# Optimization experiments

Hardware: AMD Instinct MI355X
Metric: run time of the kernel (lower is better)

Reference implementation:

```python
import jax, jax.numpy as jnp
import numpy as np

B, S, HID = 4, 2048, 1024
H, DH = 16, 64  # HID = H * DH
ADP, NTASKS = 64, 10
GATE_S = 100.0  # s (soft gate temperature), != smax=400 so no hard threshold


def setup_inputs() -> dict:
    key = jax.random.key(0)
    ks = jax.random.split(key, 13)
    sc = 0.02
    return {
        "hidden_states": jax.random.normal(ks[0], (B, S, HID), jnp.float32),
        "Wq": jax.random.normal(ks[1], (HID, HID), jnp.float32) * sc,
        "bq": jax.random.normal(ks[2], (HID,), jnp.float32) * sc,
        "Wk": jax.random.normal(ks[3], (HID, HID), jnp.float32) * sc,
        "bk": jax.random.normal(ks[4], (HID,), jnp.float32) * sc,
        "Wv": jax.random.normal(ks[5], (HID, HID), jnp.float32) * sc,
        "bv": jax.random.normal(ks[6], (HID,), jnp.float32) * sc,
        "fc1_w": jax.random.normal(ks[7], (HID, ADP), jnp.float32) * sc,
        "fc1_b": jax.random.normal(ks[8], (ADP,), jnp.float32) * sc,
        "fc2_w": jax.random.normal(ks[9], (ADP, HID), jnp.float32) * sc,
        "fc2_b": jax.random.normal(ks[10], (HID,), jnp.float32) * sc,
        "efc1": jax.random.normal(ks[11], (NTASKS, ADP), jnp.float32),
        "efc2": jax.random.normal(ks[12], (NTASKS, HID), jnp.float32),
        "t": 3,
    }


def reference(hidden_states, Wq, bq, Wk, bk, Wv, bv,
              fc1_w, fc1_b, fc2_w, fc2_b, efc1, efc2, t):
    x = hidden_states
    # --- parallel adapter with task gates (add_residual=False) ---
    gfc1 = jax.nn.sigmoid(GATE_S * efc1[t])  # [ADP]
    gfc2 = jax.nn.sigmoid(GATE_S * efc2[t])  # [HID]
    h = jax.nn.relu(x @ fc1_w + fc1_b) * gfc1          # [B,S,ADP]
    adapter_out = jax.nn.relu(h @ fc2_w + fc2_b) * gfc2  # [B,S,HID]
    # --- multi-head self-attention (absolute positions, no mask, eval dropout) ---
    def split_heads(y):  # [B,S,HID] -> [B,H,S,DH]
        return y.reshape(B, S, H, DH).transpose(0, 2, 1, 3)
    q = split_heads(x @ Wq + bq)
    k = split_heads(x @ Wk + bk)
    v = split_heads(x @ Wv + bv)
    scores = jnp.einsum("bhqd,bhkd->bhqk", q, k) / np.sqrt(DH).astype(jnp.float32)
    probs = jax.nn.softmax(scores, axis=-1)
    ctx = jnp.einsum("bhqk,bhkd->bhqd", probs, v)
    ctx = ctx.transpose(0, 2, 1, 3).reshape(B, S, HID)
    return ctx + adapter_out
```

## Files before the change

### kernel.cpp

```cpp
#include <hip/hip_runtime.h>
#include <stdint.h>
#include <stddef.h>

typedef unsigned short u16;
typedef unsigned int u32;
typedef __bf16 bf16x8 __attribute__((ext_vector_type(8)));
typedef short s16x4 __attribute__((ext_vector_type(4)));
typedef float f32x4 __attribute__((ext_vector_type(4)));

#define BB  4
#define SS  2048
#define HIDD 1024
#define NH  16
#define DHD 64

#define GLD16(gaddr, laddr) \
  __builtin_amdgcn_global_load_lds( \
      (const __attribute__((address_space(1))) u32*)(gaddr), \
      (__attribute__((address_space(3))) u32*)(laddr), 16, 0, 0)

#define LDS_BARRIER() asm volatile("s_waitcnt lgkmcnt(0)\n\ts_barrier" ::: "memory")

#if __has_builtin(__builtin_amdgcn_exp2f)
  #define EXP2(x) __builtin_amdgcn_exp2f(x)
#else
  #define EXP2(x) __expf((x) * 0.6931471805599453f)
#endif

__device__ __forceinline__ u16 f2b(float f){
  union { float f; unsigned u; } c; c.f = f;
  unsigned r = c.u + 0x7fffu + ((c.u >> 16) & 1u);
  return (u16)(r >> 16);
}
__device__ __forceinline__ u16 f2b_fast(float f){
  union { float f; unsigned u; } c; c.f = f;
  return (u16)((c.u + 0x8000u) >> 16);
}
__device__ __forceinline__ f32x4 mfma32(bf16x8 a, bf16x8 b, f32x4 c){
  return __builtin_amdgcn_mfma_f32_16x16x32_bf16(a, b, c, 0, 0, 0);
}
__device__ __forceinline__ f32x4 mfma16(s16x4 a, s16x4 b, f32x4 c){
  return __builtin_amdgcn_mfma_f32_16x16x16bf16_1k(a, b, c, 0, 0, 0);
}

__global__ __launch_bounds__(256)
void prep(const float* __restrict__ x, u16* __restrict__ xb,
          const float* __restrict__ Wq, const float* __restrict__ Wk,
          const float* __restrict__ Wv, const float* __restrict__ f1w,
          const float* __restrict__ f2w,
          u16* __restrict__ wqkv, u16* __restrict__ wtf1, u16* __restrict__ wtf2)
{
  __shared__ float tile[32][33];
  int blk = blockIdx.x;
  const int tid = threadIdx.x;
  if (blk < 8192) {
    int i = blk * 1024 + tid * 4;
    float4 v = *reinterpret_cast<const float4*>(&x[i]);
    ushort4 o;
    o.x = f2b(v.x); o.y = f2b(v.y); o.z = f2b(v.z); o.w = f2b(v.w);
    *reinterpret_cast<ushort4*>(&xb[i]) = o;
    return;
  }
  blk -= 8192;
  const float* in; u16* out; int R, C, c0, r0;
  if (blk < 3072) {
    int m = blk >> 10, t = blk & 1023;
    in = (m == 0) ? Wq : (m == 1) ? Wk : Wv;
    out = wqkv + (size_t)m * 1024 * 1024;
    R = 1024; C = 1024; c0 = (t & 31) * 32; r0 = (t >> 5) * 32;
  } else if (blk < 3136) {
    int t = blk - 3072;
    in = f1w; out = wtf1; R = 1024; C = 64;
    c0 = (t & 1) * 32; r0 = (t >> 1) * 32;
  } else {
    int t = blk - 3136;
    in = f2w; out = wtf2; R = 64; C = 1024;
    c0 = (t & 31) * 32; r0 = (t >> 5) * 32;
  }
  int tx = tid & 31, ty = tid >> 5;
  #pragma unroll
  for (int j = 0; j < 32; j += 8)
    tile[ty + j][tx] = in[(size_t)(r0 + ty + j) * C + c0 + tx];
  __syncthreads();
  #pragma unroll
  for (int j = 0; j < 32; j += 8)
    out[(size_t)(c0 + ty + j) * R + r0 + tx] = f2b(tile[tx][ty + j]);
}

__global__ __launch_bounds__(256)
void gemm_qkv(const u16* __restrict__ X, const u16* __restrict__ Wt,
              const float* __restrict__ bq, const float* __restrict__ bk,
              const float* __restrict__ bv,
              u16* __restrict__ qb, u16* __restrict__ kb, u16* __restrict__ vt)
{
  constexpr int K = 1024;
  __shared__ __align__(16) u16 ldsX[128 * 32];
  __shared__ __align__(16) u16 ldsW[128 * 32];
  const int tid = threadIdx.x;
  const int w = tid >> 6, lane = tid & 63, quad = lane >> 4, ln = lane & 15;
  const int m0 = blockIdx.y * 128, n0 = blockIdx.x * 128;
  const int wrow = (w >> 1) * 64;
  const int wcol = (w & 1) * 64;
  const int srow = tid >> 2;
  const int scol = (tid & 3) * 8;

  f32x4 acc[4][4] = {};

  for (int k0 = 0; k0 < K; k0 += 32) {
    #pragma unroll
    for (int c = 0; c < 2; ++c)
      GLD16(&X[(size_t)(m0 + c * 64 + srow) * K + k0 + scol], &ldsX[c * 2048 + w * 512]);
    #pragma unroll
    for (int c = 0; c < 2; ++c)
      GLD16(&Wt[(size_t)(n0 + c * 64 + srow) * K + k0 + scol], &ldsW[c * 2048 + w * 512]);
    __syncthreads();

    bf16x8 a[4], bfr[4];
    #pragma unroll
    for (int mt = 0; mt < 4; ++mt)
      a[mt] = *reinterpret_cast<const bf16x8*>(&ldsX[(wrow + mt * 16 + ln) * 32 + quad * 8]);
    #pragma unroll
    for (int nt = 0; nt < 4; ++nt)
      bfr[nt] = *reinterpret_cast<const bf16x8*>(&ldsW[(wcol + nt * 16 + ln) * 32 + quad * 8]);
    #pragma unroll
    for (int mt = 0; mt < 4; ++mt)
      #pragma unroll
      for (int nt = 0; nt < 4; ++nt)
        acc[mt][nt] = mfma32(a[mt], bfr[nt], acc[mt][nt]);
    __syncthreads();
  }

  if (n0 < 2048) {
    const float scale = (n0 < 1024) ? 0.18033688f : 1.f;
    const float* bias = (n0 < 1024) ? bq : bk;
    u16* dst = (n0 < 1024) ? qb : kb;
    const int nb = n0 & 1023;
    #pragma unroll
    for (int nt = 0; nt < 4; ++nt) {
      const int col = nb + wcol + nt * 16 + ln;
      const float bvv = bias[col];
      #pragma unroll
      for (int mt = 0; mt < 4; ++mt)
        #pragma unroll
        for (int r = 0; r < 4; ++r) {
          int row = m0 + wrow + mt * 16 + quad * 4 + r;
          dst[(size_t)row * 1024 + col] = f2b((acc[mt][nt][r] + bvv) * scale);
        }
    }
  } else {
    #pragma unroll
    for (int nt = 0; nt < 4; ++nt) {
      const int colv = (n0 - 2048) + wcol + nt * 16 + ln;
      const float bvv = bv[colv];
      const int h = colv >> 6, d = colv & 63;
      #pragma unroll
      for (int mt = 0; mt < 4; ++mt) {
        int row = m0 + wrow + mt * 16 + quad * 4;
        int bb = row >> 11, s = row & 2047;
        ushort4 o;
        o.x = f2b(acc[mt][nt][0] + bvv);
        o.y = f2b(acc[mt][nt][1] + bvv);
        o.z = f2b(acc[mt][nt][2] + bvv);
        o.w = f2b(acc[mt][nt][3] + bvv);
        *reinterpret_cast<ushort4*>(
            &vt[((((size_t)bb * NH + h) * DHD + d) << 11) + s]) = o;
      }
    }
  }
}

template<int BM, int BN, int WR, int WC>
__global__ __launch_bounds__(256)
void gemm_bt(const u16* __restrict__ X, const u16* __restrict__ Wt,
             const float* __restrict__ bias, u16* __restrict__ outp,
             int M, int N, int K,
             const float* __restrict__ gate, const int* __restrict__ tptr)
{
  constexpr int MT = BM / (WR * 16);
  constexpr int NT = BN / (WC * 16);
  __shared__ __align__(16) u16 ldsX[BM * 32];
  __shared__ __align__(16) u16 ldsW[BN * 32];
  const int tid = threadIdx.x;
  const int w = tid >> 6, lane = tid & 63, quad = lane >> 4, ln = lane & 15;
  const int m0 = blockIdx.y * BM, n0 = blockIdx.x * BN;
  const int wrow = (w / WC) * (MT * 16);
  const int wcol = (w % WC) * (NT * 16);
  const int srow = tid >> 2;
  const int scol = (tid & 3) * 8;

  f32x4 acc[MT][NT] = {};

  for (int k0 = 0; k0 < K; k0 += 32) {
    #pragma unroll
    for (int c = 0; c < BM / 64; ++c)
      GLD16(&X[(size_t)(m0 + c * 64 + srow) * K + k0 + scol], &ldsX[c * 2048 + w * 512]);
    #pragma unroll
    for (int c = 0; c < BN / 64; ++c)
      GLD16(&Wt[(size_t)(n0 + c * 64 + srow) * K + k0 + scol], &ldsW[c * 2048 + w * 512]);
    __syncthreads();

    bf16x8 a[MT], bfr[NT];
    #pragma unroll
    for (int mt = 0; mt < MT; ++mt)
      a[mt] = *reinterpret_cast<const bf16x8*>(&ldsX[(wrow + mt * 16 + ln) * 32 + quad * 8]);
    #pragma unroll
    for (int nt = 0; nt < NT; ++nt)
      bfr[nt] = *reinterpret_cast<const bf16x8*>(&ldsW[(wcol + nt * 16 + ln) * 32 + quad * 8]);
    #pragma unroll
    for (int mt = 0; mt < MT; ++mt)
      #pragma unroll
      for (int nt = 0; nt < NT; ++nt)
        acc[mt][nt] = mfma32(a[mt], bfr[nt], acc[mt][nt]);
    __syncthreads();
  }

  int t = tptr[0];
  if ((unsigned)t > 9u) t = 0;
  #pragma unroll
  for (int nt = 0; nt < NT; ++nt) {
    const int col = n0 + wcol + nt * 16 + ln;
    const float bvv = bias[col];
    const float g = 1.f / (1.f + __expf(-100.f * gate[t * N + col]));
    #pragma unroll
    for (int mt = 0; mt < MT; ++mt) {
      #pragma unroll
      for (int r = 0; r < 4; ++r) {
        int row = m0 + wrow + mt * 16 + quad * 4 + r;
        outp[(size_t)row * N + col] = f2b(fmaxf(acc[mt][nt][r] + bvv, 0.f) * g);
      }
    }
  }
}

__global__ __launch_bounds__(256, 4)
void attn(const u16* __restrict__ Q, const u16* __restrict__ Kb,
          const u16* __restrict__ Vt, const u16* __restrict__ hb,
          const u16* __restrict__ w2, const float* __restrict__ b2,
          const float* __restrict__ gate2, const int* __restrict__ tptr,
          float* __restrict__ out)
{
  __shared__ __align__(16) u16 ldsK[64 * 72];
  __shared__ __align__(16) u16 ldsV[64 * 76];

  const int tid = threadIdx.x;
  const int w = tid >> 6, lane = tid & 63, quad = lane >> 4, ln = lane & 15;
  const int h = blockIdx.x, b = blockIdx.y, qt = blockIdx.z;
  const int bh = b * NH + h;
  const int qbase = qt * 128 + w * 32;
  const int skey = tid >> 3;
  const int sd   = (tid & 7) * 8;

  bf16x8 qf[2][2];
  #pragma unroll
  for (int q2 = 0; q2 < 2; ++q2)
    #pragma unroll
    for (int kk = 0; kk < 2; ++kk)
      qf[q2][kk] = *reinterpret_cast<const bf16x8*>(
          &Q[(size_t)(b * SS + qbase + q2 * 16 + ln) * HIDD + h * DHD + kk * 32 + quad * 8]);

  f32x4 o[4][2] = {};
  float lsum[2] = {0.f, 0.f};

  const u16* Kp = &Kb[(size_t)(b * SS + skey) * HIDD + h * DHD + sd];
  const u16* Vp = &Vt[((size_t)bh * DHD + skey) * SS + sd];

  uint4 rK0 = *reinterpret_cast<const uint4*>(Kp);
  uint4 rK1 = *reinterpret_cast<const uint4*>(Kp + (size_t)32 * HIDD);
  uint4 rV0 = *reinterpret_cast<const uint4*>(Vp);
  uint4 rV1 = *reinterpret_cast<const uint4*>(Vp + (size_t)32 * SS);

  for (int kt = 0; kt < SS; kt += 64) {
    LDS_BARRIER();
    *reinterpret_cast<uint4*>(&ldsK[skey * 72 + sd])        = rK0;
    *reinterpret_cast<uint4*>(&ldsK[(32 + skey) * 72 + sd]) = rK1;
    *reinterpret_cast<uint4*>(&ldsV[skey * 76 + sd])        = rV0;
    *reinterpret_cast<uint4*>(&ldsV[(32 + skey) * 76 + sd]) = rV1;
    if (kt + 64 < SS) {
      const u16* Kn = Kp + (size_t)(kt + 64) * HIDD;
      const u16* Vn = Vp + (kt + 64);
      rK0 = *reinterpret_cast<const uint4*>(Kn);
      rK1 = *reinterpret_cast<const uint4*>(Kn + (size_t)32 * HIDD);
      rV0 = *reinterpret_cast<const uint4*>(Vn);
      rV1 = *reinterpret_cast<const uint4*>(Vn + (size_t)32 * SS);
    }
    LDS_BARRIER();

    f32x4 s[4][2];
    #pragma unroll
    for (int k4 = 0; k4 < 4; ++k4) {
      bf16x8 kf0 = *reinterpret_cast<const bf16x8*>(&ldsK[(k4 * 16 + ln) * 72 + quad * 8]);
      bf16x8 kf1 = *reinterpret_cast<const bf16x8*>(&ldsK[(k4 * 16 + ln) * 72 + 32 + quad * 8]);
      #pragma unroll
      for (int q2 = 0; q2 < 2; ++q2) {
        f32x4 z = {0.f, 0.f, 0.f, 0.f};
        z = mfma32(kf0, qf[q2][0], z);
        z = mfma32(kf1, qf[q2][1], z);
        s[k4][q2] = z;
      }
    }

    s16x4 p[4][2];
    #pragma unroll
    for (int k4 = 0; k4 < 4; ++k4)
      #pragma unroll
      for (int q2 = 0; q2 < 2; ++q2)
        #pragma unroll
        for (int r = 0; r < 4; ++r) {
          float pv = EXP2(s[k4][q2][r]);
          lsum[q2] += pv;
          p[k4][q2][r] = (short)f2b_fast(pv);
        }

    #pragma unroll
    for (int dt = 0; dt < 4; ++dt) {
      #pragma unroll
      for (int ks = 0; ks < 4; ++ks) {
        s16x4 vf = *reinterpret_cast<const s16x4*>(
            &ldsV[(dt * 16 + ln) * 76 + ks * 16 + quad * 4]);
        #pragma unroll
        for (int q2 = 0; q2 < 2; ++q2)
          o[dt][q2] = mfma16(vf, p[ks][q2], o[dt][q2]);
      }
    }
  }

  float rl[2];
  #pragma unroll
  for (int q2 = 0; q2 < 2; ++q2) {
    float v = lsum[q2];
    v += __shfl_xor(v, 16);
    v += __shfl_xor(v, 32);
    rl[q2] = 1.f / v;
  }

  f32x4 acc2[4][2] = {};
  #pragma unroll
  for (int kk = 0; kk < 2; ++kk) {
    bf16x8 hf[2];
    #pragma unroll
    for (int q2 = 0; q2 < 2; ++q2) {
      int q = qbase + q2 * 16 + ln;
      hf[q2] = *reinterpret_cast<const bf16x8*>(
          &hb[(size_t)(b * SS + q) * 64 + kk * 32 + quad * 8]);
    }
    #pragma unroll
    for (int dt = 0; dt < 4; ++dt) {
      bf16x8 wf = *reinterpret_cast<const bf16x8*>(
          &w2[(size_t)(h * DHD + dt * 16 + ln) * 64 + kk * 32 + quad * 8]);
      #pragma unroll
      for (int q2 = 0; q2 < 2; ++q2)
        acc2[dt][q2] = mfma32(wf, hf[q2], acc2[dt][q2]);
    }
  }

  int t = tptr[0];
  if ((unsigned)t > 9u) t = 0;
  float bv2[4][4], gv2[4][4];
  #pragma unroll
  for (int dt = 0; dt < 4; ++dt)
    #pragma unroll
    for (int r = 0; r < 4; ++r) {
      int col = h * DHD + dt * 16 + quad * 4 + r;
      bv2[dt][r] = b2[col];
      gv2[dt][r] = 1.f / (1.f + __expf(-100.f * gate2[t * HIDD + col]));
    }

  #pragma unroll
  for (int q2 = 0; q2 < 2; ++q2) {
    const int q = qbase + q2 * 16 + ln;
    float* orow = &out[(size_t)(b * SS + q) * HIDD + h * DHD];
    #pragma unroll
    for (int dt = 0; dt < 4; ++dt)
      #pragma unroll
      for (int r = 0; r < 4; ++r) {
        int d = dt * 16 + quad * 4 + r;
        float ad = fmaxf(acc2[dt][q2][r] + bv2[dt][r], 0.f) * gv2[dt][r];
        orow[d] = o[dt][q2][r] * rl[q2] + ad;
      }
  }
}

extern "C" void kernel_launch(void* const* d_in, const int* in_sizes, int n_in,
                              void* d_out, int out_size, void* d_ws, size_t ws_size,
                              hipStream_t stream) {
  const float* x    = (const float*)d_in[0];
  const float* Wq   = (const float*)d_in[1];
  const float* bq   = (const float*)d_in[2];
  const float* Wk   = (const float*)d_in[3];
  const float* bk   = (const float*)d_in[4];
  const float* Wv   = (const float*)d_in[5];
  const float* bv   = (const float*)d_in[6];
  const float* f1w  = (const float*)d_in[7];
  const float* f1b  = (const float*)d_in[8];
  const float* f2w  = (const float*)d_in[9];
  const float* f2b_ = (const float*)d_in[10];
  const float* efc1 = (const float*)d_in[11];
  const float* efc2 = (const float*)d_in[12];
  const int*   tptr = (const int*)d_in[13];
  float* out = (float*)d_out;

  unsigned char* ws = (unsigned char*)d_ws;
  u16* xb   = (u16*)(ws + 0);
  u16* wqkv = (u16*)(ws + (16u << 20));
  u16* wtf1 = (u16*)(ws + (22u << 20));
  u16* wtf2 = (u16*)(ws + (22u << 20) + (128u << 10));
  u16* hb   = (u16*)(ws + (23u << 20));
  u16* qb   = (u16*)(ws + (24u << 20));
  u16* kb   = (u16*)(ws + (40u << 20));
  u16* vt   = (u16*)(ws + (56u << 20));

  prep<<<dim3(11392), 256, 0, stream>>>(x, xb, Wq, Wk, Wv, f1w, f2w,
                                        wqkv, wtf1, wtf2);

  gemm_qkv<<<dim3(24, 64), 256, 0, stream>>>(xb, wqkv, bq, bk, bv, qb, kb, vt);

  gemm_bt<64,64,2,2><<<dim3(1, 128), 256, 0, stream>>>(
      xb, wtf1, f1b, hb, 8192, 64, 1024, efc1, tptr);

  attn<<<dim3(NH, BB, SS / 128), 256, 0, stream>>>(
      qb, kb, vt, hb, wtf2, f2b_, efc2, tptr, out);
}
```

Measured before the change: 289.9 us.

## Fuse adapter fc1 into QKV GEMM and halve attention query tile per block

```diff
diff --git a/kernel.cpp b/kernel.cpp
--- a/kernel.cpp
+++ b/kernel.cpp
@@ -5,6 +5,7 @@
 typedef unsigned short u16;
 typedef unsigned int u32;
 typedef __bf16 bf16x8 __attribute__((ext_vector_type(8)));
+typedef __bf16 bf16x4 __attribute__((ext_vector_type(4)));
 typedef short s16x4 __attribute__((ext_vector_type(4)));
 typedef float f32x4 __attribute__((ext_vector_type(4)));
 
@@ -31,10 +32,6 @@
   union { float f; unsigned u; } c; c.f = f;
   unsigned r = c.u + 0x7fffu + ((c.u >> 16) & 1u);
   return (u16)(r >> 16);
-}
-__device__ __forceinline__ u16 f2b_fast(float f){
-  union { float f; unsigned u; } c; c.f = f;
-  return (u16)((c.u + 0x8000u) >> 16);
 }
 __device__ __forceinline__ f32x4 mfma32(bf16x8 a, bf16x8 b, f32x4 c){
   return __builtin_amdgcn_mfma_f32_16x16x32_bf16(a, b, c, 0, 0, 0);
@@ -62,6 +59,12 @@
     return;
   }
   blk -= 8192;
+  if (blk >= 3200) {
+    u16* pad = wqkv + (size_t)3136 * 1024;
+    uint4 z = make_uint4(0u, 0u, 0u, 0u);
+    *reinterpret_cast<uint4*>(&pad[(size_t)(blk - 3200) * 2048 + tid * 8]) = z;
+    return;
+  }
   const float* in; u16* out; int R, C, c0, r0;
   if (blk < 3072) {
     int m = blk >> 10, t = blk & 1023;
@@ -91,7 +94,10 @@
 void gemm_qkv(const u16* __restrict__ X, const u16* __restrict__ Wt,
               const float* __restrict__ bq, const float* __restrict__ bk,
               const float* __restrict__ bv,
-              u16* __restrict__ qb, u16* __restrict__ kb, u16* __restrict__ vt)
+              const float* __restrict__ f1b, const float* __restrict__ efc1,
+              const int* __restrict__ tptr,
+              u16* __restrict__ qb, u16* __restrict__ kb, u16* __restrict__ vt,
+              u16* __restrict__ hb)
 {
   constexpr int K = 1024;
   __shared__ __align__(16) u16 ldsX[128 * 32];
@@ -147,7 +153,7 @@
           dst[(size_t)row * 1024 + col] = f2b((acc[mt][nt][r] + bvv) * scale);
         }
     }
-  } else {
+  } else if (n0 < 3072) {
     #pragma unroll
     for (int nt = 0; nt < 4; ++nt) {
       const int colv = (n0 - 2048) + wcol + nt * 16 + ln;
@@ -166,73 +172,26 @@
             &vt[((((size_t)bb * NH + h) * DHD + d) << 11) + s]) = o;
       }
     }
-  }
-}
-
-template<int BM, int BN, int WR, int WC>
-__global__ __launch_bounds__(256)
-void gemm_bt(const u16* __restrict__ X, const u16* __restrict__ Wt,
-             const float* __restrict__ bias, u16* __restrict__ outp,
-             int M, int N, int K,
-             const float* __restrict__ gate, const int* __restrict__ tptr)
-{
-  constexpr int MT = BM / (WR * 16);
-  constexpr int NT = BN / (WC * 16);
-  __shared__ __align__(16) u16 ldsX[BM * 32];
-  __shared__ __align__(16) u16 ldsW[BN * 32];
-  const int tid = threadIdx.x;
-  const int w = tid >> 6, lane = tid & 63, quad = lane >> 4, ln = lane & 15;
-  const int m0 = blockIdx.y * BM, n0 = blockIdx.x * BN;
-  const int wrow = (w / WC) * (MT * 16);
-  const int wcol = (w % WC) * (NT * 16);
-  const int srow = tid >> 2;
-  const int scol = (tid & 3) * 8;
-
-  f32x4 acc[MT][NT] = {};
-
-  for (int k0 = 0; k0 < K; k0 += 32) {
-    #pragma unroll
-    for (int c = 0; c < BM / 64; ++c)
-      GLD16(&X[(size_t)(m0 + c * 64 + srow) * K + k0 + scol], &ldsX[c * 2048 + w * 512]);
-    #pragma unroll
-    for (int c = 0; c < BN / 64; ++c)
-      GLD16(&Wt[(size_t)(n0 + c * 64 + srow) * K + k0 + scol], &ldsW[c * 2048 + w * 512]);
-    __syncthreads();
-
-    bf16x8 a[MT], bfr[NT];
-    #pragma unroll
-    for (int mt = 0; mt < MT; ++mt)
-      a[mt] = *reinterpret_cast<const bf16x8*>(&ldsX[(wrow + mt * 16 + ln) * 32 + quad * 8]);
-    #pragma unroll
-    for (int nt = 0; nt < NT; ++nt)
-      bfr[nt] = *reinterpret_cast<const bf16x8*>(&ldsW[(wcol + nt * 16 + ln) * 32 + quad * 8]);
-    #pragma unroll
-    for (int mt = 0; mt < MT; ++mt)
-      #pragma unroll
-      for (int nt = 0; nt < NT; ++nt)
-        acc[mt][nt] = mfma32(a[mt], bfr[nt], acc[mt][nt]);
-    __syncthreads();
-  }
-
-  int t = tptr[0];
-  if ((unsigned)t > 9u) t = 0;
-  #pragma unroll
-  for (int nt = 0; nt < NT; ++nt) {
-    const int col = n0 + wcol + nt * 16 + ln;
-    const float bvv = bias[col];
-    const float g = 1.f / (1.f + __expf(-100.f * gate[t * N + col]));
-    #pragma unroll
-    for (int mt = 0; mt < MT; ++mt) {
-      #pragma unroll
-      for (int r = 0; r < 4; ++r) {
-        int row = m0 + wrow + mt * 16 + quad * 4 + r;
-        outp[(size_t)row * N + col] = f2b(fmaxf(acc[mt][nt][r] + bvv, 0.f) * g);
-      }
-    }
-  }
-}
-
-__global__ __launch_bounds__(256, 4)
+  } else if (wcol == 0) {
+    int t = tptr[0];
+    if ((unsigned)t > 9u) t = 0;
+    #pragma unroll
+    for (int nt = 0; nt < 4; ++nt) {
+      const int col = nt * 16 + ln;
+      const float bvv = f1b[col];
+      const float g = 1.f / (1.f + __expf(-100.f * efc1[t * 64 + col]));
+      #pragma unroll
+      for (int mt = 0; mt < 4; ++mt)
+        #pragma unroll
+        for (int r = 0; r < 4; ++r) {
+          int row = m0 + wrow + mt * 16 + quad * 4 + r;
+          hb[(size_t)row * 64 + col] = f2b(fmaxf(acc[mt][nt][r] + bvv, 0.f) * g);
+        }
+    }
+  }
+}
+
+__global__ __launch_bounds__(256, 8)
 void attn(const u16* __restrict__ Q, const u16* __restrict__ Kb,
           const u16* __restrict__ Vt, const u16* __restrict__ hb,
           const u16* __restrict__ w2, const float* __restrict__ b2,
@@ -246,20 +205,18 @@
   const int w = tid >> 6, lane = tid & 63, quad = lane >> 4, ln = lane & 15;
   const int h = blockIdx.x, b = blockIdx.y, qt = blockIdx.z;
   const int bh = b * NH + h;
-  const int qbase = qt * 128 + w * 32;
+  const int qbase = qt * 64 + w * 16;
   const int skey = tid >> 3;
   const int sd   = (tid & 7) * 8;
 
-  bf16x8 qf[2][2];
-  #pragma unroll
-  for (int q2 = 0; q2 < 2; ++q2)
-    #pragma unroll
-    for (int kk = 0; kk < 2; ++kk)
-      qf[q2][kk] = *reinterpret_cast<const bf16x8*>(
-          &Q[(size_t)(b * SS + qbase + q2 * 16 + ln) * HIDD + h * DHD + kk * 32 + quad * 8]);
-
-  f32x4 o[4][2] = {};
-  float lsum[2] = {0.f, 0.f};
+  bf16x8 qf[2];
+  #pragma unroll
+  for (int kk = 0; kk < 2; ++kk)
+    qf[kk] = *reinterpret_cast<const bf16x8*>(
+        &Q[(size_t)(b * SS + qbase + ln) * HIDD + h * DHD + kk * 32 + quad * 8]);
+
+  f32x4 o[4] = {};
+  float lsum = 0.f;
 
   const u16* Kp = &Kb[(size_t)(b * SS + skey) * HIDD + h * DHD + sd];
   const u16* Vp = &Vt[((size_t)bh * DHD + skey) * SS + sd];
@@ -285,99 +242,77 @@
     }
     LDS_BARRIER();
 
-    f32x4 s[4][2];
+    f32x4 s[4];
+    __builtin_amdgcn_s_setprio(1);
     #pragma unroll
     for (int k4 = 0; k4 < 4; ++k4) {
       bf16x8 kf0 = *reinterpret_cast<const bf16x8*>(&ldsK[(k4 * 16 + ln) * 72 + quad * 8]);
       bf16x8 kf1 = *reinterpret_cast<const bf16x8*>(&ldsK[(k4 * 16 + ln) * 72 + 32 + quad * 8]);
-      #pragma unroll
-      for (int q2 = 0; q2 < 2; ++q2) {
-        f32x4 z = {0.f, 0.f, 0.f, 0.f};
-        z = mfma32(kf0, qf[q2][0], z);
-        z = mfma32(kf1, qf[q2][1], z);
-        s[k4][q2] = z;
+      f32x4 z = {0.f, 0.f, 0.f, 0.f};
+      z = mfma32(kf0, qf[0], z);
+      z = mfma32(kf1, qf[1], z);
+      s[k4] = z;
+    }
+    __builtin_amdgcn_s_setprio(0);
+
+    s16x4 p[4];
+    #pragma unroll
+    for (int k4 = 0; k4 < 4; ++k4) {
+      union { bf16x4 b; s16x4 s; } cv;
+      #pragma unroll
+      for (int r = 0; r < 4; ++r) {
+        float pv = EXP2(s[k4][r]);
+        lsum += pv;
+        cv.b[r] = (__bf16)pv;
       }
-    }
-
-    s16x4 p[4][2];
-    #pragma unroll
-    for (int k4 = 0; k4 < 4; ++k4)
-      #pragma unroll
-      for (int q2 = 0; q2 < 2; ++q2)
-        #pragma unroll
-        for (int r = 0; r < 4; ++r) {
-          float pv = EXP2(s[k4][q2][r]);
-          lsum[q2] += pv;
-          p[k4][q2][r] = (short)f2b_fast(pv);
-        }
-
+      p[k4] = cv.s;
+    }
+
+    __builtin_amdgcn_s_setprio(1);
     #pragma unroll
     for (int dt = 0; dt < 4; ++dt) {
       #pragma unroll
       for (int ks = 0; ks < 4; ++ks) {
         s16x4 vf = *reinterpret_cast<const s16x4*>(
             &ldsV[(dt * 16 + ln) * 76 + ks * 16 + quad * 4]);
-        #pragma unroll
-        for (int q2 = 0; q2 < 2; ++q2)
-          o[dt][q2] = mfma16(vf, p[ks][q2], o[dt][q2]);
+        o[dt] = mfma16(vf, p[ks], o[dt]);
       }
     }
-  }
-
-  float rl[2];
-  #pragma unroll
-  for (int q2 = 0; q2 < 2; ++q2) {
-    float v = lsum[q2];
-    v += __shfl_xor(v, 16);
-    v += __shfl_xor(v, 32);
-    rl[q2] = 1.f / v;
-  }
-
-  f32x4 acc2[4][2] = {};
+    __builtin_amdgcn_s_setprio(0);
+  }
+
+  float v = lsum;
+  v += __shfl_xor(v, 16);
+  v += __shfl_xor(v, 32);
+  const float rl = 1.f / v;
+
+  f32x4 acc2[4] = {};
   #pragma unroll
   for (int kk = 0; kk < 2; ++kk) {
-    bf16x8 hf[2];
-    #pragma unroll
-    for (int q2 = 0; q2 < 2; ++q2) {
-      int q = qbase + q2 * 16 + ln;
-      hf[q2] = *reinterpret_cast<const bf16x8*>(
-          &hb[(size_t)(b * SS + q) * 64 + kk * 32 + quad * 8]);
-    }
+    bf16x8 hf = *reinterpret_cast<const bf16x8*>(
+        &hb[(size_t)(b * SS + qbase + ln) * 64 + kk * 32 + quad * 8]);
     #pragma unroll
     for (int dt = 0; dt < 4; ++dt) {
       bf16x8 wf = *reinterpret_cast<const bf16x8*>(
           &w2[(size_t)(h * DHD + dt * 16 + ln) * 64 + kk * 32 + quad * 8]);
-      #pragma unroll
-      for (int q2 = 0; q2 < 2; ++q2)
-        acc2[dt][q2] = mfma32(wf, hf[q2], acc2[dt][q2]);
+      acc2[dt] = mfma32(wf, hf, acc2[dt]);
     }
   }
 
   int t = tptr[0];
   if ((unsigned)t > 9u) t = 0;
-  float bv2[4][4], gv2[4][4];
+  const int q = qbase + ln;
+  float* orow = &out[(size_t)(b * SS + q) * HIDD + h * DHD];
   #pragma unroll
   for (int dt = 0; dt < 4; ++dt)
     #pragma unroll
     for (int r = 0; r < 4; ++r) {
-      int col = h * DHD + dt * 16 + quad * 4 + r;
-      bv2[dt][r] = b2[col];
-      gv2[dt][r] = 1.f / (1.f + __expf(-100.f * gate2[t * HIDD + col]));
-    }
-
-  #pragma unroll
-  for (int q2 = 0; q2 < 2; ++q2) {
-    const int q = qbase + q2 * 16 + ln;
-    float* orow = &out[(size_t)(b * SS + q) * HIDD + h * DHD];
-    #pragma unroll
-    for (int dt = 0; dt < 4; ++dt)
-      #pragma unroll
-      for (int r = 0; r < 4; ++r) {
-        int d = dt * 16 + quad * 4 + r;
-        float ad = fmaxf(acc2[dt][q2][r] + bv2[dt][r], 0.f) * gv2[dt][r];
-        orow[d] = o[dt][q2][r] * rl[q2] + ad;
-      }
-  }
+      int d = dt * 16 + quad * 4 + r;
+      int col = h * DHD + d;
+      float g2 = 1.f / (1.f + __expf(-100.f * gate2[t * HIDD + col]));
+      float ad = fmaxf(acc2[dt][r] + b2[col], 0.f) * g2;
+      orow[d] = o[dt][r] * rl + ad;
+    }
 }
 
 extern "C" void kernel_launch(void* const* d_in, const int* in_sizes, int n_in,
@@ -402,21 +337,19 @@
   unsigned char* ws = (unsigned char*)d_ws;
   u16* xb   = (u16*)(ws + 0);
   u16* wqkv = (u16*)(ws + (16u << 20));
-  u16* wtf1 = (u16*)(ws + (22u << 20));
-  u16* wtf2 = (u16*)(ws + (22u << 20) + (128u << 10));
+  u16* wtf1 = wqkv + (size_t)3072 * 1024;
+  u16* wtf2 = (u16*)(ws + (22u << 20) + (256u << 10));
   u16* hb   = (u16*)(ws + (23u << 20));
   u16* qb   = (u16*)(ws + (24u << 20));
   u16* kb   = (u16*)(ws + (40u << 20));
   u16* vt   = (u16*)(ws + (56u << 20));
 
-  prep<<<dim3(11392), 256, 0, stream>>>(x, xb, Wq, Wk, Wv, f1w, f2w,
+  prep<<<dim3(11424), 256, 0, stream>>>(x, xb, Wq, Wk, Wv, f1w, f2w,
                                         wqkv, wtf1, wtf2);
 
-  gemm_qkv<<<dim3(24, 64), 256, 0, stream>>>(xb, wqkv, bq, bk, bv, qb, kb, vt);
-
-  gemm_bt<64,64,2,2><<<dim3(1, 128), 256, 0, stream>>>(
-      xb, wtf1, f1b, hb, 8192, 64, 1024, efc1, tptr);
-
-  attn<<<dim3(NH, BB, SS / 128), 256, 0, stream>>>(
+  gemm_qkv<<<dim3(25, 64), 256, 0, stream>>>(xb, wqkv, bq, bk, bv,
+                                             f1b, efc1, tptr, qb, kb, vt, hb);
+
+  attn<<<dim3(NH, BB, SS / 64), 256, 0, stream>>>(
       qb, kb, vt, hb, wtf2, f2b_, efc2, tptr, out);
 }
```

Measured after the change: 448.8 us. 54.8% more time.
